# Optimization experiments

Hardware: AMD Instinct MI355X
Metric: run time of the kernel (lower is better)

Reference implementation:

```python
import jax, jax.numpy as jnp
import numpy as np

B, S, D = 16, 2048, 128

def setup_inputs() -> dict:
    key = jax.random.key(0)
    k1, k2, k3 = jax.random.split(key, 3)
    return {
        "query": jax.random.normal(k1, (B, S, D), dtype=jnp.float32),
        "key": jax.random.normal(k2, (B, S, D), dtype=jnp.float32),
        "value": jax.random.normal(k3, (B, S, D), dtype=jnp.float32),
    }

def reference(query, key, value):
    dq = query.shape[-1]
    dk = key.shape[-1]
    # custom scale: sqrt(Dq) + sqrt(Dk - Dq); with Dq == Dk this is sqrt(Dq)
    inv_scale = np.sqrt(dq) + np.sqrt(dk - dq)
    qk = jnp.einsum("bqd,bkd->bqk", query, key) / jnp.float32(inv_scale)
    attn = jax.nn.softmax(qk, axis=-1)  # dropout_p=0 -> identity
    return jnp.einsum("bqk,bkd->bqd", attn, value)
```

## Files before the change

### kernel.cpp

```cpp
#include <hip/hip_runtime.h>
#include <stdint.h>

#define Bn 16
#define Sn 2048
#define Dn 128
#define QBLK 128
#define KVBLK 64
#define NTHR 512
#define NT (Sn / KVBLK)

typedef __attribute__((ext_vector_type(4))) float f32x4;
typedef __attribute__((ext_vector_type(16))) float f32x16;
typedef __attribute__((ext_vector_type(8))) short bf16x8;
typedef __attribute__((ext_vector_type(2))) unsigned int u32x2;

#define BUFSZ 32768
#define SMEM_BYTES 67584

__device__ __forceinline__ uint32_t f2bf_u(float f) {
  return (__float_as_uint(f) + 0x8000u) >> 16;
}
__device__ __forceinline__ uint32_t pk2(float a, float b) {
  return f2bf_u(a) | (f2bf_u(b) << 16);
}

__global__ __launch_bounds__(256) void tr_kv(const float* __restrict__ K,
                                             const float* __restrict__ V,
                                             unsigned short* __restrict__ Kf,
                                             unsigned short* __restrict__ Vf) {
  __shared__ unsigned short lds[64 * 136];
  const int tid = threadIdx.x;
  const size_t tileoff = (size_t)blockIdx.x * (64 * Dn);

  {
    const float* src = K + tileoff;
#pragma unroll
    for (int it = 0; it < 8; ++it) {
      const int gr = it * 256 + tid;
      const int k = gr >> 5, g4 = gr & 31;
      const float4 v = ((const float4*)src)[gr];
      unsigned short* p = &lds[k * 136 + g4 * 4];
      p[0] = (unsigned short)f2bf_u(v.x);
      p[1] = (unsigned short)f2bf_u(v.y);
      p[2] = (unsigned short)f2bf_u(v.z);
      p[3] = (unsigned short)f2bf_u(v.w);
    }
    __syncthreads();
    char* dst = (char*)Kf + (size_t)blockIdx.x * 16384;
#pragma unroll
    for (int it = 0; it < 4; ++it) {
      const int g = it * 256 + tid;
      const int lane = g & 63, dk = (g >> 6) & 7, h = g >> 9;
      const unsigned short* p =
          &lds[(32 * h + (lane & 31)) * 136 + dk * 16 + 8 * (lane >> 5)];
      uint4 o;
      o.x = (uint32_t)p[0] | ((uint32_t)p[1] << 16);
      o.y = (uint32_t)p[2] | ((uint32_t)p[3] << 16);
      o.z = (uint32_t)p[4] | ((uint32_t)p[5] << 16);
      o.w = (uint32_t)p[6] | ((uint32_t)p[7] << 16);
      *(uint4*)(dst + g * 16) = o;
    }
  }
  __syncthreads();

  {
    const float* src = V + tileoff;
#pragma unroll
    for (int it = 0; it < 8; ++it) {
      const int gr = it * 256 + tid;
      const int k = gr >> 5, g4 = gr & 31;
      const float4 v = ((const float4*)src)[gr];
      unsigned short* p = &lds[k * 136 + g4 * 4];
      p[0] = (unsigned short)f2bf_u(v.x);
      p[1] = (unsigned short)f2bf_u(v.y);
      p[2] = (unsigned short)f2bf_u(v.z);
      p[3] = (unsigned short)f2bf_u(v.w);
    }
    __syncthreads();
    char* dst = (char*)Vf + (size_t)blockIdx.x * 16384;
#pragma unroll
    for (int it = 0; it < 4; ++it) {
      const int g = it * 256 + tid;
      const int lane = g & 63, f3 = (g >> 6) & 7, h = g >> 9;
      const int d = (f3 >> 1) * 32 + (lane & 31);
      const int k0 = 32 * h + (f3 & 1) * 16 + 8 * (lane >> 5);
      uint4 o;
      o.x = (uint32_t)lds[(k0 + 0) * 136 + d] | ((uint32_t)lds[(k0 + 1) * 136 + d] << 16);
      o.y = (uint32_t)lds[(k0 + 2) * 136 + d] | ((uint32_t)lds[(k0 + 3) * 136 + d] << 16);
      o.z = (uint32_t)lds[(k0 + 4) * 136 + d] | ((uint32_t)lds[(k0 + 5) * 136 + d] << 16);
      o.w = (uint32_t)lds[(k0 + 6) * 136 + d] | ((uint32_t)lds[(k0 + 7) * 136 + d] << 16);
      *(uint4*)(dst + g * 16) = o;
    }
  }
}

__global__ __launch_bounds__(NTHR, 2) void attn_fwd(
    const float* __restrict__ Q, const unsigned short* __restrict__ Kf,
    const unsigned short* __restrict__ Vf, float* __restrict__ O) {
  __shared__ uint4 smem_[SMEM_BYTES / 16];
  char* smem = (char*)smem_;

  const int tid = threadIdx.x;
  const int lane = tid & 63;
  const int w = tid >> 6;
  const int qw = w & 3;
  const int h = w >> 2;
  const int hi = lane >> 5;
  const int ql = lane & 31;

  const int i = blockIdx.x;
  const int j = i >> 3;
  const int b = (i & 7) + 8 * (j & 1);
  const int q0 = (j >> 1) * QBLK;
  const int qg = q0 + qw * 32 + ql;

  const float qscale = 0.08838834764831845f * 1.44269504088896340736f;
  bf16x8 qf[8];
  {
    const float* qrow = Q + (size_t)(b * Sn + qg) * Dn;
#pragma unroll
    for (int dk = 0; dk < 8; ++dk) {
      const int d0 = dk * 16 + hi * 8;
      const float4 a = *(const float4*)(qrow + d0);
      const float4 d = *(const float4*)(qrow + d0 + 4);
      bf16x8 q8;
      q8[0] = (short)f2bf_u(a.x * qscale); q8[1] = (short)f2bf_u(a.y * qscale);
      q8[2] = (short)f2bf_u(a.z * qscale); q8[3] = (short)f2bf_u(a.w * qscale);
      q8[4] = (short)f2bf_u(d.x * qscale); q8[5] = (short)f2bf_u(d.y * qscale);
      q8[6] = (short)f2bf_u(d.z * qscale); q8[7] = (short)f2bf_u(d.w * qscale);
      qf[dk] = q8;
    }
  }

  f32x16 o[4];
#pragma unroll
  for (int dt = 0; dt < 4; ++dt) {
#pragma unroll
    for (int jj = 0; jj < 16; ++jj) o[dt][jj] = 0.f;
  }
  float l_r = 0.f;

  const char* Kg = (const char*)(Kf + (size_t)b * Sn * Dn);
  const char* Vg = (const char*)(Vf + (size_t)b * Sn * Dn);

#define STAGE(dst_, t_)                                                        \
  {                                                                            \
    const char* gk = Kg + (size_t)(t_)*16384 + w * 2048 + lane * 16;           \
    const char* gv = Vg + (size_t)(t_)*16384 + w * 2048 + lane * 16;           \
    char* lk = smem + (dst_) + w * 2048;                                       \
    char* lv = smem + (dst_) + 16384 + w * 2048;                               \
    _Pragma("unroll") for (int it = 0; it < 2; ++it) {                         \
      __builtin_amdgcn_global_load_lds(                                        \
          (const __attribute__((address_space(1))) uint32_t*)(gk + it * 1024), \
          (__attribute__((address_space(3))) uint32_t*)(lk + it * 1024),       \
          16, 0, 0);                                                           \
      __builtin_amdgcn_global_load_lds(                                        \
          (const __attribute__((address_space(1))) uint32_t*)(gv + it * 1024), \
          (__attribute__((address_space(3))) uint32_t*)(lv + it * 1024),       \
          16, 0, 0);                                                           \
    }                                                                          \
  }

#define LOADVF(vd_, cb_)                                                       \
  {                                                                            \
    const char* vt = smem + (cb_) + 16384 + h * 8192 + lane * 16;              \
    _Pragma("unroll") for (int f = 0; f < 8; ++f)                              \
        vd_[f] = *(const bf16x8*)(vt + f * 1024);                              \
  }

#define QKT(sd_, cb_)                                                          \
  {                                                                            \
    _Pragma("unroll") for (int jj = 0; jj < 16; ++jj) sd_[jj] = -8.0f;         \
    const char* kt = smem + (cb_) + h * 8192 + lane * 16;                      \
    __builtin_amdgcn_s_setprio(1);                                             \
    _Pragma("unroll") for (int dk = 0; dk < 8; ++dk) {                         \
      bf16x8 kfr = *(const bf16x8*)(kt + dk * 1024);                           \
      sd_ = __builtin_amdgcn_mfma_f32_32x32x16_bf16(kfr, qf[dk], sd_, 0, 0, 0);\
    }                                                                          \
    __builtin_amdgcn_s_setprio(0);                                             \
  }

#define SOFTPV(s_, vf_)                                                        \
  {                                                                            \
    _Pragma("unroll") for (int jj = 0; jj < 16; ++jj)                          \
        s_[jj] = __builtin_amdgcn_exp2f(s_[jj]);                               \
    {                                                                          \
      float r0 = 0.f, r1 = 0.f, r2 = 0.f, r3 = 0.f;                            \
      _Pragma("unroll") for (int jj = 0; jj < 4; ++jj) {                       \
        r0 += s_[jj]; r1 += s_[4 + jj]; r2 += s_[8 + jj]; r3 += s_[12 + jj];   \
      }                                                                        \
      l_r += (r0 + r1) + (r2 + r3);      \
    }                                                                          \
    uint32_t own[4][2];                                                        \
    _Pragma("unroll") for (int mm = 0; mm < 4; ++mm) {                         \
      own[mm][0] = pk2(s_[4 * mm + 0], s_[4 * mm + 1]);                        \
      own[mm][1] = pk2(s_[4 * mm + 2], s_[4 * mm + 3]);                        \
    }                                                                          \
    uint32_t rcv[2][2];                                                        \
    _Pragma("unroll") for (int jj = 0; jj < 2; ++jj)                           \
        _Pragma("unroll") for (int e = 0; e < 2; ++e) {                        \
      uint32_t sel = hi ? own[2 * jj][e] : own[2 * jj + 1][e];                 \
      rcv[jj][e] = (uint32_t)__shfl_xor((int)sel, 32, 64);                     \
    }                                                                          \
    bf16x8 pb[2];                                                              \
    _Pragma("unroll") for (int ks = 0; ks < 2; ++ks) {                         \
      union { uint32_t u[4]; bf16x8 v; } tt;                                   \
      tt.u[0] = hi ? rcv[ks][0] : own[2 * ks][0];                              \
      tt.u[1] = hi ? rcv[ks][1] : own[2 * ks][1];                              \
      tt.u[2] = hi ? own[2 * ks + 1][0] : rcv[ks][0];                          \
      tt.u[3] = hi ? own[2 * ks + 1][1] : rcv[ks][1];                          \
      pb[ks] = tt.v;                                                           \
    }                                                                          \
    __builtin_amdgcn_s_setprio(1);                                             \
    _Pragma("unroll") for (int dt = 0; dt < 4; ++dt) {                         \
      _Pragma("unroll") for (int ks = 0; ks < 2; ++ks) {                       \
        o[dt] = __builtin_amdgcn_mfma_f32_32x32x16_bf16(vf_[dt * 2 + ks],      \
                                                        pb[ks], o[dt], 0, 0, 0);\
      }                                                                        \
    }                                                                          \
    __builtin_amdgcn_s_setprio(0);                                             \
  }

  bf16x8 vA[8];
  f32x16 sA, sB;
  STAGE(0, 0)
  __syncthreads();
  STAGE(BUFSZ, 1)
  QKT(sA, 0)
  for (int t = 0; t < NT; t += 2) {
    LOADVF(vA, 0)
    __syncthreads();
    if (t + 2 < NT) STAGE(0, t + 2)
    if (t + 1 < NT) QKT(sB, BUFSZ)
    SOFTPV(sA, vA)
    LOADVF(vA, BUFSZ)
    __syncthreads();
    if (t + 3 < NT) STAGE(BUFSZ, t + 3)
    if (t + 2 < NT) QKT(sA, 0)
    SOFTPV(sB, vA)
  }

  l_r += __shfl_xor(l_r, 32, 64);
  char* xch = smem + qw * 16896;
  if (h) {
#pragma unroll
    for (int dt = 0; dt < 4; ++dt) {
#pragma unroll
      for (int q2 = 0; q2 < 4; ++q2) {
        float4 v;
        v.x = o[dt][4 * q2 + 0]; v.y = o[dt][4 * q2 + 1];
        v.z = o[dt][4 * q2 + 2]; v.w = o[dt][4 * q2 + 3];
        *(float4*)(xch + (dt * 4 + q2) * 1024 + lane * 16) = v;
      }
    }
    *(float*)(xch + 16384 + lane * 4) = l_r;
  }
  __syncthreads();
  if (!h) {
    const float l1 = *(const float*)(xch + 16384 + lane * 4);
    const float inv = 1.0f / (l_r + l1);
    float* orow = O + (size_t)(b * Sn + qg) * Dn;
#pragma unroll
    for (int dt = 0; dt < 4; ++dt) {
#pragma unroll
      for (int q2 = 0; q2 < 4; ++q2) {
        const float4 o1v =
            *(const float4*)(xch + (dt * 4 + q2) * 1024 + lane * 16);
        float4 v;
        v.x = (o[dt][4 * q2 + 0] + o1v.x) * inv;
        v.y = (o[dt][4 * q2 + 1] + o1v.y) * inv;
        v.z = (o[dt][4 * q2 + 2] + o1v.z) * inv;
        v.w = (o[dt][4 * q2 + 3] + o1v.w) * inv;
        *(float4*)(orow + dt * 32 + q2 * 8 + hi * 4) = v;
      }
    }
  }
}

extern "C" void kernel_launch(void* const* d_in, const int* in_sizes, int n_in,
                              void* d_out, int out_size, void* d_ws, size_t ws_size,
                              hipStream_t stream) {
  (void)in_sizes; (void)n_in; (void)out_size; (void)ws_size;
  const float* Q = (const float*)d_in[0];
  const float* K = (const float*)d_in[1];
  const float* V = (const float*)d_in[2];
  float* O = (float*)d_out;

  const size_t nE = (size_t)Bn * Sn * Dn;
  unsigned short* Kf = (unsigned short*)d_ws;
  unsigned short* Vf = Kf + nE;

  tr_kv<<<dim3(Bn * 32, 1, 1), dim3(256, 1, 1), 0, stream>>>(K, V, Kf, Vf);
  attn_fwd<<<dim3((Sn / QBLK) * Bn, 1, 1), dim3(NTHR, 1, 1), 0, stream>>>(
      Q, Kf, Vf, O);
}
```

Before: 58.30 us.

## Stage KV tiles in pairs with 64KB double buffers and one barrier per pair

Each pipeline step now covers two KV tiles (128 keys). K and V for both tiles are loaded into a 64KB half of a 128KB LDS double buffer, and the next pair is prefetched while the current one is processed. The two QK^T MFMA chains are interleaved within each step, and only one __syncthreads is issued per pair instead of one per tile. The cost is twice the LDS footprint, which can limit how many workgroups fit per CU, and QK^T no longer overlaps with the previous tile's softmax/PV work.

```diff
diff --git a/kernel.cpp b/kernel.cpp
--- a/kernel.cpp
+++ b/kernel.cpp
@@ -8,14 +8,15 @@
 #define KVBLK 64
 #define NTHR 512
 #define NT (Sn / KVBLK)
+#define NP (NT / 2)
 
 typedef __attribute__((ext_vector_type(4))) float f32x4;
 typedef __attribute__((ext_vector_type(16))) float f32x16;
 typedef __attribute__((ext_vector_type(8))) short bf16x8;
 typedef __attribute__((ext_vector_type(2))) unsigned int u32x2;
 
-#define BUFSZ 32768
-#define SMEM_BYTES 67584
+#define PBUF 65536
+#define SMEM_BYTES 131072
 
 __device__ __forceinline__ uint32_t f2bf_u(float f) {
   return (__float_as_uint(f) + 0x8000u) >> 16;
@@ -143,13 +144,13 @@
   const char* Kg = (const char*)(Kf + (size_t)b * Sn * Dn);
   const char* Vg = (const char*)(Vf + (size_t)b * Sn * Dn);
 
-#define STAGE(dst_, t_)                                                        \
+#define STAGE2(dst_, p_)                                                       \
   {                                                                            \
-    const char* gk = Kg + (size_t)(t_)*16384 + w * 2048 + lane * 16;           \
-    const char* gv = Vg + (size_t)(t_)*16384 + w * 2048 + lane * 16;           \
-    char* lk = smem + (dst_) + w * 2048;                                       \
-    char* lv = smem + (dst_) + 16384 + w * 2048;                               \
-    _Pragma("unroll") for (int it = 0; it < 2; ++it) {                         \
+    const char* gk = Kg + (size_t)(p_)*32768 + w * 4096 + lane * 16;           \
+    const char* gv = Vg + (size_t)(p_)*32768 + w * 4096 + lane * 16;           \
+    char* lk = smem + (dst_) + w * 4096;                                       \
+    char* lv = smem + (dst_) + 32768 + w * 4096;                               \
+    _Pragma("unroll") for (int it = 0; it < 4; ++it) {                         \
       __builtin_amdgcn_global_load_lds(                                        \
           (const __attribute__((address_space(1))) uint32_t*)(gk + it * 1024), \
           (__attribute__((address_space(3))) uint32_t*)(lk + it * 1024),       \
@@ -161,23 +162,11 @@
     }                                                                          \
   }
 
-#define LOADVF(vd_, cb_)                                                       \
+#define LOADVF(vd_, vb_)                                                       \
   {                                                                            \
-    const char* vt = smem + (cb_) + 16384 + h * 8192 + lane * 16;              \
+    const char* vt = smem + (vb_) + h * 8192 + lane * 16;                      \
     _Pragma("unroll") for (int f = 0; f < 8; ++f)                              \
         vd_[f] = *(const bf16x8*)(vt + f * 1024);                              \
-  }
-
-#define QKT(sd_, cb_)                                                          \
-  {                                                                            \
-    _Pragma("unroll") for (int jj = 0; jj < 16; ++jj) sd_[jj] = -8.0f;         \
-    const char* kt = smem + (cb_) + h * 8192 + lane * 16;                      \
-    __builtin_amdgcn_s_setprio(1);                                             \
-    _Pragma("unroll") for (int dk = 0; dk < 8; ++dk) {                         \
-      bf16x8 kfr = *(const bf16x8*)(kt + dk * 1024);                           \
-      sd_ = __builtin_amdgcn_mfma_f32_32x32x16_bf16(kfr, qf[dk], sd_, 0, 0, 0);\
-    }                                                                          \
-    __builtin_amdgcn_s_setprio(0);                                             \
   }
 
 #define SOFTPV(s_, vf_)                                                        \
@@ -221,23 +210,37 @@
     __builtin_amdgcn_s_setprio(0);                                             \
   }
 
-  bf16x8 vA[8];
-  f32x16 sA, sB;
-  STAGE(0, 0)
+  STAGE2(0, 0)
   __syncthreads();
-  STAGE(BUFSZ, 1)
-  QKT(sA, 0)
-  for (int t = 0; t < NT; t += 2) {
-    LOADVF(vA, 0)
+  for (int p = 0; p < NP; ++p) {
+    const uint32_t cb = (uint32_t)(p & 1) * PBUF;
+    if (p + 1 < NP) STAGE2(PBUF - cb, p + 1)
+    __builtin_amdgcn_sched_barrier(0);
+
+    f32x16 sA, sB;
+#pragma unroll
+    for (int jj = 0; jj < 16; ++jj) { sA[jj] = -8.0f; sB[jj] = -8.0f; }
+    {
+      const char* kt0 = smem + cb + h * 8192 + lane * 16;
+      const char* kt1 = smem + cb + 16384 + h * 8192 + lane * 16;
+      __builtin_amdgcn_s_setprio(1);
+#pragma unroll
+      for (int dk = 0; dk < 8; ++dk) {
+        bf16x8 k0 = *(const bf16x8*)(kt0 + dk * 1024);
+        bf16x8 k1 = *(const bf16x8*)(kt1 + dk * 1024);
+        sA = __builtin_amdgcn_mfma_f32_32x32x16_bf16(k0, qf[dk], sA, 0, 0, 0);
+        sB = __builtin_amdgcn_mfma_f32_32x32x16_bf16(k1, qf[dk], sB, 0, 0, 0);
+      }
+      __builtin_amdgcn_s_setprio(0);
+    }
+
+    bf16x8 vA[8];
+    LOADVF(vA, cb + 32768)
+    SOFTPV(sA, vA)
+    LOADVF(vA, cb + 49152)
+    SOFTPV(sB, vA)
+
     __syncthreads();
-    if (t + 2 < NT) STAGE(0, t + 2)
-    if (t + 1 < NT) QKT(sB, BUFSZ)
-    SOFTPV(sA, vA)
-    LOADVF(vA, BUFSZ)
-    __syncthreads();
-    if (t + 3 < NT) STAGE(BUFSZ, t + 3)
-    if (t + 2 < NT) QKT(sA, 0)
-    SOFTPV(sB, vA)
   }
 
   l_r += __shfl_xor(l_r, 32, 64);
```

Result: faster. 56.83 us, median of 2 (-2.5%).
